# Kernel optimization log

Measured on AMD Instinct MI355X. Metric: run time of the kernel, lower is better.

Reference implementation:

```python
import jax, jax.numpy as jnp
import numpy as np

TAU = 2.0       # LIF membrane time constant (spikingjelly default)
ALPHA = 2.0     # ATan surrogate sharpness
EPS = 1e-5      # BN eps
NUM_HEADS = 12
PATCH = 2
LENTH = 256     # (H/PATCH)*(W/PATCH)

@jax.custom_vjp
def heaviside(x):
    return (x >= 0.0).astype(x.dtype)

def _hv_fwd(x):
    return heaviside(x), x

def _hv_bwd(x, g):
    sg = ALPHA / 2.0 / (1.0 + (jnp.pi / 2.0 * ALPHA * x) ** 2)  # ATan surrogate
    return (g * sg,)

heaviside.defvjp(_hv_fwd, _hv_bwd)

def lif(x):
    # multi-step LIF over leading time axis, hard reset, v_th = 1.0
    def step(v, xt):
        v = v + (xt - v) / TAU
        s = heaviside(v - 1.0)
        return v * (1.0 - s), s
    _, s = jax.lax.scan(step, jnp.zeros_like(x[0]), x)
    return s

def setup_inputs() -> dict:
    key = jax.random.key(0)
    ks = jax.random.split(key, 9)
    T, B, C, H, W = 4, 4, 384, 32, 32
    x = jax.random.normal(ks[0], (T, B, C, H, W), dtype=jnp.float32)
    Wconv = jax.random.normal(ks[1], (2 * C, C, PATCH, PATCH), dtype=jnp.float32) * (1.0 / np.sqrt(C * PATCH * PATCH))
    gamma1 = jax.random.uniform(ks[2], (2 * C,), dtype=jnp.float32, minval=0.5, maxval=1.5)
    beta1 = jax.random.normal(ks[3], (2 * C,), dtype=jnp.float32) * 0.1
    Wproj = jax.random.normal(ks[4], (C, C), dtype=jnp.float32) * (1.0 / np.sqrt(C))
    gamma2 = jax.random.uniform(ks[5], (C,), dtype=jnp.float32, minval=0.5, maxval=1.5)
    beta2 = jax.random.normal(ks[6], (C,), dtype=jnp.float32) * 0.1
    firing_rate_x = jax.random.uniform(ks[7], (1, 1, NUM_HEADS, 1, 1), dtype=jnp.float32, minval=0.05, maxval=0.5)
    firing_rate_attn = jax.random.uniform(ks[8], (1, 1, NUM_HEADS, 1, 1), dtype=jnp.float32, minval=0.05, maxval=0.5)
    return {"x": x, "Wconv": Wconv, "gamma1": gamma1, "beta1": beta1, "Wproj": Wproj,
            "gamma2": gamma2, "beta2": beta2, "firing_rate_x": firing_rate_x,
            "firing_rate_attn": firing_rate_attn}

def reference(x, Wconv, gamma1, beta1, Wproj, gamma2, beta2, firing_rate_x, firing_rate_attn):
    T, B, C, H, W = x.shape
    d = C // NUM_HEADS
    xs = lif(x)                                          # spikes [T,B,C,H,W]
    # patch conv dim -> 2*dim, stride = kernel = PATCH (eval BN: running mean 0, var 1)
    y = jax.lax.conv_general_dilated(xs.reshape(T * B, C, H, W), Wconv,
                                     (PATCH, PATCH), 'VALID',
                                     dimension_numbers=('NCHW', 'OIHW', 'NCHW'))
    bn1 = gamma1 / jnp.sqrt(1.0 + EPS)
    y = y * bn1[None, :, None, None] + beta1[None, :, None, None]
    Np = (H // PATCH) * (W // PATCH)                     # == LENTH
    y = y.reshape(T, B, NUM_HEADS, 2 * d, Np)
    y1, y2 = y[:, :, :, :d, :], y[:, :, :, d:, :]
    xr = xs.reshape(T, B, NUM_HEADS, d, H * W)
    scale1 = 1.0 / jnp.sqrt(firing_rate_x * d)
    attn = jnp.einsum('tbhdn,tbhdm->tbhnm', y1, xr) * scale1   # [T,B,h,Np,HW]
    attn = lif(attn)
    scale2 = 1.0 / jnp.sqrt(firing_rate_attn * LENTH)
    out = jnp.einsum('tbhdn,tbhnm->tbhdm', y2, attn) * scale2  # [T,B,h,d,HW]
    out = out.reshape(T, B, C, H, W)
    out = lif(out)
    out = jnp.einsum('oc,tbchw->tbohw', Wproj, out)            # 1x1 conv proj
    bn2 = gamma2 / jnp.sqrt(1.0 + EPS)
    out = out * bn2[None, None, :, None, None] + beta2[None, None, :, None, None]
    return out + x
```

## Files before the change

kernel.cpp:

```cpp
#include <hip/hip_runtime.h>
#include <hip/hip_bf16.h>
#include <math.h>


typedef __attribute__((ext_vector_type(8))) short short8;
typedef __attribute__((ext_vector_type(4))) float f32x4;

#define T_ 4
#define B_ 4
#define C_ 384
#define HW 1024
#define NH_ 12
#define Np_ 256
#define EPS_ 1e-5f
#define LDK 56

static __device__ __forceinline__ unsigned short f2bf(float f) {
    __hip_bfloat16 h = __float2bfloat16(f);
    return *reinterpret_cast<unsigned short*>(&h);
}
static __device__ __forceinline__ float bf2f(unsigned short u) {
    __hip_bfloat16 h = *reinterpret_cast<__hip_bfloat16*>(&u);
    return __bfloat162float(h);
}
static __device__ __forceinline__ void split3(float w, unsigned short& u0,
                                              unsigned short& u1, unsigned short& u2) {
    u0 = f2bf(w);  float f0 = bf2f(u0);
    float r1 = w - f0;
    u1 = f2bf(r1); float f1 = bf2f(u1);
    u2 = f2bf(r1 - f1);
}

__global__ __launch_bounds__(256) void k_wsplit(const float* __restrict__ Wc,
                                                const float* __restrict__ Wp,
                                                unsigned short* __restrict__ Wc3,
                                                unsigned short* __restrict__ Wp3) {
    const int NC = 768 * 1536;
    const int NP = 384 * 384;
    int i = blockIdx.x * 256 + threadIdx.x;
    float w; unsigned short* dst; int idx, plane;
    if (i < NC) { w = Wc[i]; dst = Wc3; idx = i; plane = NC; }
    else {
        int j = i - NC;
        if (j >= NP) return;
        w = Wp[j]; dst = Wp3; idx = j; plane = NP;
    }
    unsigned short u0, u1, u2;
    split3(w, u0, u1, u2);
    dst[idx] = u0; dst[plane + idx] = u1; dst[2 * plane + idx] = u2;
}

__global__ __launch_bounds__(256) void k_lif_im2col(const float* __restrict__ x,
                                                    unsigned short* __restrict__ Bc,
                                                    unsigned short* __restrict__ xsb) {
    int gt = blockIdx.x * 256 + threadIdx.x;
    int pw = gt & 15, ph = (gt >> 4) & 15;
    int v = gt >> 8;
    int c = v % 384, b = v / 384;
    float v00 = 0.f, v01 = 0.f, v10 = 0.f, v11 = 0.f;
    const size_t xrow = ((size_t)b * C_ + c) * HW + (size_t)(2 * ph) * 32 + 2 * pw;
#pragma unroll
    for (int t = 0; t < T_; ++t) {
        const float* px = x + (size_t)t * (B_ * C_ * HW) + xrow;
        float2 r0 = *(const float2*)px;
        float2 r1 = *(const float2*)(px + 32);
        v00 += (r0.x - v00) * 0.5f;
        v01 += (r0.y - v01) * 0.5f;
        v10 += (r1.x - v10) * 0.5f;
        v11 += (r1.y - v11) * 0.5f;
        ushort4 s;
        s.x = (v00 >= 1.f) ? 0x3F80 : 0; if (v00 >= 1.f) v00 = 0.f;
        s.y = (v01 >= 1.f) ? 0x3F80 : 0; if (v01 >= 1.f) v01 = 0.f;
        s.z = (v10 >= 1.f) ? 0x3F80 : 0; if (v10 >= 1.f) v10 = 0.f;
        s.w = (v11 >= 1.f) ? 0x3F80 : 0; if (v11 >= 1.f) v11 = 0.f;
        int tb = t * B_ + b;
        int n = tb * 256 + ph * 16 + pw;
        *(ushort4*)(Bc + (size_t)n * 1536 + 4 * c) = s;
        size_t xo = ((size_t)tb * C_ + c) * HW + (size_t)(2 * ph) * 32 + 2 * pw;
        ushort2 w0 = {s.x, s.y}, w1 = {s.z, s.w};
        *(ushort2*)(xsb + xo) = w0;
        *(ushort2*)(xsb + xo + 32) = w1;
    }
}

#define GL16(GP, LP) __builtin_amdgcn_global_load_lds(                        \
    (const __attribute__((address_space(1))) void*)(GP),                      \
    (__attribute__((address_space(3))) void*)(LP), 16, 0, 0)

static __device__ __forceinline__ void stage_conv(const unsigned short* __restrict__ Wc3,
                                                  const unsigned short* __restrict__ Bc,
                                                  short* smb, int mb, int nb, int k0,
                                                  int wid, int rloc, int cswz) {
    if (wid == 0) {
#pragma unroll
        for (int s = 0; s < 3; ++s)
#pragma unroll
            for (int u = 0; u < 2; ++u)
                GL16(Wc3 + ((size_t)(s * 768 + mb * 32 + u * 16 + rloc)) * 1536 + k0 + cswz * 8,
                     smb + s * 1024 + u * 512);
        GL16(Bc + ((size_t)(nb * 128 + rloc)) * 1536 + k0 + cswz * 8, smb + 3072);
    } else {
#pragma unroll
        for (int v = 1; v < 8; ++v)
            GL16(Bc + ((size_t)(nb * 128 + v * 16 + rloc)) * 1536 + k0 + cswz * 8,
                 smb + 3072 + v * 512);
    }
}

__global__ __launch_bounds__(128) void k_mconv(const unsigned short* __restrict__ Bc,
                                               const unsigned short* __restrict__ Wc3,
                                               const float* __restrict__ g1,
                                               const float* __restrict__ b1,
                                               const float* __restrict__ frx,
                                               const float* __restrict__ fra,
                                               unsigned short* __restrict__ y1s,
                                               unsigned short* __restrict__ y2s) {
    __shared__ short sm[2][7168];
    const int nb = blockIdx.x, mb = blockIdx.y;
    const int tid = threadIdx.x;
    const int lane = tid & 63, wid = tid >> 6;
    const int quad = lane >> 4, lr = lane & 15;
    const int rloc = lane >> 2;
    const int cswz = (lane & 3) ^ ((lane >> 3) & 3);
    const int slot = quad ^ ((lr >> 1) & 3);
    const int wn = wid;

    f32x4 acc[2][4];
#pragma unroll
    for (int im = 0; im < 2; ++im)
#pragma unroll
        for (int in = 0; in < 4; ++in)
            acc[im][in] = (f32x4){0.f, 0.f, 0.f, 0.f};

    stage_conv(Wc3, Bc, sm[0], mb, nb, 0, wid, rloc, cswz);

#pragma unroll 2
    for (int kt = 0; kt < 48; ++kt) {
        const int b = kt & 1;
        if (kt < 47) {
            stage_conv(Wc3, Bc, sm[b ^ 1], mb, nb, (kt + 1) * 32, wid, rloc, cswz);
            asm volatile("s_waitcnt vmcnt(7)" ::: "memory");
        } else {
            asm volatile("s_waitcnt vmcnt(0)" ::: "memory");
        }
        __builtin_amdgcn_s_barrier();
        __builtin_amdgcn_sched_barrier(0);

        const short* smb = sm[b];
        short8 af[3][2], bf[4];
#pragma unroll
        for (int s = 0; s < 3; ++s)
#pragma unroll
            for (int im = 0; im < 2; ++im)
                af[s][im] = *(const short8*)&smb[s * 1024 + (im * 16 + lr) * 32 + slot * 8];
#pragma unroll
        for (int in = 0; in < 4; ++in)
            bf[in] = *(const short8*)&smb[3072 + (wn * 64 + in * 16 + lr) * 32 + slot * 8];
        asm volatile("s_waitcnt lgkmcnt(0)" ::: "memory");
        __builtin_amdgcn_sched_barrier(0);
        __builtin_amdgcn_s_barrier();
        __builtin_amdgcn_sched_barrier(0);

#pragma unroll
        for (int s = 0; s < 3; ++s)
#pragma unroll
            for (int im = 0; im < 2; ++im)
#pragma unroll
                for (int in = 0; in < 4; ++in)
                    acc[im][in] = __builtin_amdgcn_mfma_f32_16x16x32_bf16(af[s][im], bf[in], acc[im][in], 0, 0, 0);
    }

    const float rs = 1.0f / sqrtf(1.0f + EPS_);
    const int h = mb >> 1, half = mb & 1;
    const float scl = (half == 0) ? (1.0f / sqrtf(frx[h] * 32.0f))
                                  : (1.0f / sqrtf(fra[h] * 256.0f));
    unsigned short* dst = (half == 0) ? y1s : y2s;
#pragma unroll
    for (int im = 0; im < 2; ++im) {
#pragma unroll
        for (int in = 0; in < 4; ++in) {
            int n_g = nb * 128 + wn * 64 + in * 16 + lr;
            int tb = n_g >> 8, pn = n_g & 255;
            size_t base = (size_t)(tb * NH_ + h) * 3 * 8192;
            ushort4 o0, o1, o2;
#pragma unroll
            for (int r = 0; r < 4; ++r) {
                int oc = mb * 32 + im * 16 + quad * 4 + r;
                float val = (acc[im][in][r] * (g1[oc] * rs) + b1[oc]) * scl;
                unsigned short u0, u1, u2;
                split3(val, u0, u1, u2);
                ((unsigned short*)&o0)[r] = u0;
                ((unsigned short*)&o1)[r] = u1;
                ((unsigned short*)&o2)[r] = u2;
            }
            int dd = im * 16 + quad * 4;
            if (half == 0) {
                *(ushort4*)&dst[base + 0 * 8192 + (size_t)pn * 32 + dd] = o0;
                *(ushort4*)&dst[base + 1 * 8192 + (size_t)pn * 32 + dd] = o1;
                *(ushort4*)&dst[base + 2 * 8192 + (size_t)pn * 32 + dd] = o2;
            } else {
#pragma unroll
                for (int r = 0; r < 4; ++r) {
                    dst[base + 0 * 8192 + (size_t)(dd + r) * 256 + pn] = ((unsigned short*)&o0)[r];
                    dst[base + 1 * 8192 + (size_t)(dd + r) * 256 + pn] = ((unsigned short*)&o1)[r];
                    dst[base + 2 * 8192 + (size_t)(dd + r) * 256 + pn] = ((unsigned short*)&o2)[r];
                }
            }
        }
    }
}

__global__ __launch_bounds__(256, 2) void k_attn_qk(const unsigned short* __restrict__ xsb,
                                                    const unsigned short* __restrict__ y1s,
                                                    unsigned short* __restrict__ abq) {
    __shared__ unsigned short xb[4][64][40];
    const int h = blockIdx.y, b = blockIdx.z;
    const int tid = threadIdx.x;
    const int lane = tid & 63, wq = tid >> 6;
    const int quad = lane >> 4, lr = lane & 15;
    const int m0 = blockIdx.x * 64;

#pragma unroll
    for (int i = 0; i < 8; ++i) {
        int e = tid + i * 256;
        int j4 = e & 15, d = (e >> 4) & 31, t = e >> 9;
        ushort4 v = *(const ushort4*)(xsb + ((size_t)((t * B_ + b) * C_) + h * 32 + d) * HW + m0 + j4 * 4);
        xb[t][j4 * 4 + 0][d] = v.x;
        xb[t][j4 * 4 + 1][d] = v.y;
        xb[t][j4 * 4 + 2][d] = v.z;
        xb[t][j4 * 4 + 3][d] = v.w;
    }
    __syncthreads();

    float vat[4][4][4];
#pragma unroll
    for (int mi = 0; mi < 4; ++mi)
#pragma unroll
        for (int itl = 0; itl < 4; ++itl)
#pragma unroll
            for (int r = 0; r < 4; ++r) vat[mi][itl][r] = 0.f;

#pragma unroll
    for (int t = 0; t < T_; ++t) {
        const int tb = t * B_ + b;
        const size_t slab = (size_t)(tb * NH_ + h) * 3 * 8192;

        short8 af[3][4];
        const unsigned short* y1p = y1s + slab + (size_t)(wq * 64 + lr) * 32 + quad * 8;
#pragma unroll
        for (int s = 0; s < 3; ++s)
#pragma unroll
            for (int itl = 0; itl < 4; ++itl)
                af[s][itl] = *(const short8*)(y1p + s * 8192 + itl * 512);

#pragma unroll
        for (int mi = 0; mi < 4; ++mi) {
            short8 bx = *(const short8*)&xb[t][mi * 16 + lr][quad * 8];
            f32x4 acc[4];
#pragma unroll
            for (int itl = 0; itl < 4; ++itl) acc[itl] = (f32x4){0.f, 0.f, 0.f, 0.f};
#pragma unroll
            for (int s = 0; s < 3; ++s)
#pragma unroll
                for (int itl = 0; itl < 4; ++itl)
                    acc[itl] = __builtin_amdgcn_mfma_f32_16x16x32_bf16(af[s][itl], bx, acc[itl], 0, 0, 0);

            unsigned int q = 0;
#pragma unroll
            for (int itl = 0; itl < 4; ++itl)
#pragma unroll
                for (int r = 0; r < 4; ++r) {
                    float v = vat[mi][itl][r];
                    v += (acc[itl][r] - v) * 0.5f;
                    bool s = (v >= 1.0f);
                    vat[mi][itl][r] = s ? 0.f : v;
                    q |= (s ? 1u : 0u) << (itl * 4 + r);
                }
            int m = m0 + mi * 16 + lr;
            abq[(((size_t)(tb * NH_ + h) * 1024 + m) * 4 + quad) * 4 + wq] = (unsigned short)q;
        }
    }
}

__global__ __launch_bounds__(128) void k_attn_pv(const unsigned long long* __restrict__ abits,
                                                 const unsigned short* __restrict__ y2s,
                                                 unsigned short* __restrict__ obt) {
    const int h = blockIdx.y, b = blockIdx.z;
    const int tid = threadIdx.x;
    const int lane = tid & 63;
    const int quad = lane >> 4, lr = lane & 15;
    const int dt = tid >> 6;
    const int mbase = blockIdx.x * 64;
    const int obase = (quad & 2) << 1;

    float vo[4][4];
#pragma unroll
    for (int mi = 0; mi < 4; ++mi)
#pragma unroll
        for (int r = 0; r < 4; ++r) vo[mi][r] = 0.f;

#pragma unroll
    for (int t = 0; t < T_; ++t) {
        const int tb = t * B_ + b;
        const size_t slab = (size_t)(tb * NH_ + h) * 3 * 8192;

        short8 ay[3][8];
        const unsigned short* y2p = y2s + slab + (size_t)(dt * 16 + lr) * 256 + quad * 8;
#pragma unroll
        for (int s = 0; s < 3; ++s)
#pragma unroll
            for (int kt = 0; kt < 8; ++kt)
                ay[s][kt] = *(const short8*)(y2p + s * 8192 + kt * 32);

#pragma unroll
        for (int mi = 0; mi < 4; ++mi) {
            const int m = mbase + mi * 16 + lr;
            const unsigned long long* ap = abits + ((size_t)(tb * NH_ + h) * 1024 + m) * 4 + (quad & 1) * 2;
            unsigned long long Qa = ap[0];
            unsigned long long Qb = ap[1];

            short8 bs[8];
#pragma unroll
            for (int kt = 0; kt < 8; ++kt) {
                int o = kt * 8 + obase;
                unsigned int a4 = (unsigned int)(Qa >> o) & 15u;
                unsigned int b4 = (unsigned int)(Qb >> o) & 15u;
                union { short8 v; unsigned int w[4]; } u;
                u.w[0] = ((a4 & 1u) ? 0x3F80u : 0u) | ((a4 & 2u) ? 0x3F800000u : 0u);
                u.w[1] = ((a4 & 4u) ? 0x3F80u : 0u) | ((a4 & 8u) ? 0x3F800000u : 0u);
                u.w[2] = ((b4 & 1u) ? 0x3F80u : 0u) | ((b4 & 2u) ? 0x3F800000u : 0u);
                u.w[3] = ((b4 & 4u) ? 0x3F80u : 0u) | ((b4 & 8u) ? 0x3F800000u : 0u);
                bs[kt] = u.v;
            }

            f32x4 acc2 = (f32x4){0.f, 0.f, 0.f, 0.f};
#pragma unroll
            for (int s = 0; s < 3; ++s)
#pragma unroll
                for (int kt = 0; kt < 8; ++kt)
                    acc2 = __builtin_amdgcn_mfma_f32_16x16x32_bf16(ay[s][kt], bs[kt], acc2, 0, 0, 0);

            ushort4 ob;
#pragma unroll
            for (int r = 0; r < 4; ++r) {
                float v = vo[mi][r];
                v += (acc2[r] - v) * 0.5f;
                bool s = (v >= 1.0f);
                ((unsigned short*)&ob)[r] = s ? 0x3F80 : 0;
                vo[mi][r] = s ? 0.f : v;
            }
            *(ushort4*)(obt + ((size_t)tb * HW + m) * C_ + h * 32 + dt * 16 + quad * 4) = ob;
        }
    }
}

__global__ __launch_bounds__(256) void k_mproj(const unsigned short* __restrict__ obt,
                                               const unsigned short* __restrict__ Wp3,
                                               const float* __restrict__ g2,
                                               const float* __restrict__ b2,
                                               const float* __restrict__ x,
                                               float* __restrict__ out) {
    __shared__ short As[3][64][LDK];
    __shared__ short Bs[128][LDK];
    const int nb = blockIdx.x, mb = blockIdx.y;
    const int tid = threadIdx.x;
    const int lane = tid & 63, wave = tid >> 6;
    const int wm = wave >> 1, wn = wave & 1;
    const int quad = lane >> 4, lr = lane & 15;
    const int arow = tid >> 2, akoff = (tid & 3) * 8;
    f32x4 acc[2][4];
#pragma unroll
    for (int im = 0; im < 2; ++im)
#pragma unroll
        for (int in = 0; in < 4; ++in)
            acc[im][in] = (f32x4){0.f, 0.f, 0.f, 0.f};

    for (int k0 = 0; k0 < 384; k0 += 32) {
#pragma unroll
        for (int s = 0; s < 3; ++s) {
            short8 a = *(const short8*)(Wp3 + ((size_t)(s * 384 + mb * 64 + arow)) * 384 + k0 + akoff);
            *(short8*)&As[s][arow][akoff] = a;
        }
#pragma unroll
        for (int i = 0; i < 2; ++i) {
            int f = i * 256 + tid;
            int row = f >> 2, koff = (f & 3) * 8;
            short8 bv = *(const short8*)(obt + ((size_t)(nb * 128 + row)) * 384 + k0 + koff);
            *(short8*)&Bs[row][koff] = bv;
        }
        __syncthreads();
        short8 bf[4], af[3][2];
#pragma unroll
        for (int in = 0; in < 4; ++in)
            bf[in] = *(const short8*)&Bs[wn * 64 + in * 16 + lr][quad * 8];
#pragma unroll
        for (int s = 0; s < 3; ++s)
#pragma unroll
            for (int im = 0; im < 2; ++im)
                af[s][im] = *(const short8*)&As[s][wm * 32 + im * 16 + lr][quad * 8];
#pragma unroll
        for (int s = 0; s < 3; ++s)
#pragma unroll
            for (int im = 0; im < 2; ++im)
#pragma unroll
                for (int in = 0; in < 4; ++in)
                    acc[im][in] = __builtin_amdgcn_mfma_f32_16x16x32_bf16(af[s][im], bf[in], acc[im][in], 0, 0, 0);
        __syncthreads();
    }
    const float rs = 1.0f / sqrtf(1.0f + EPS_);
#pragma unroll
    for (int im = 0; im < 2; ++im) {
#pragma unroll
        for (int in = 0; in < 4; ++in) {
            int n_g = nb * 128 + wn * 64 + in * 16 + lr;
            int tb = n_g >> 10, hw = n_g & 1023;
#pragma unroll
            for (int r = 0; r < 4; ++r) {
                int o = mb * 64 + wm * 32 + im * 16 + quad * 4 + r;
                size_t idx = ((size_t)tb * C_ + o) * HW + hw;
                out[idx] = acc[im][in][r] * (g2[o] * rs) + b2[o] + x[idx];
            }
        }
    }
}

extern "C" void kernel_launch(void* const* d_in, const int* in_sizes, int n_in,
                              void* d_out, int out_size, void* d_ws, size_t ws_size,
                              hipStream_t stream) {
    const float* x      = (const float*)d_in[0];
    const float* Wconv  = (const float*)d_in[1];
    const float* gamma1 = (const float*)d_in[2];
    const float* beta1  = (const float*)d_in[3];
    const float* Wproj  = (const float*)d_in[4];
    const float* gamma2 = (const float*)d_in[5];
    const float* beta2  = (const float*)d_in[6];
    const float* frx    = (const float*)d_in[7];
    const float* fra    = (const float*)d_in[8];
    float* out = (float*)d_out;

    unsigned short* ws16 = (unsigned short*)d_ws;
    unsigned short* Bc  = ws16;
    unsigned short* obt = ws16;
    unsigned short* Wc3 = ws16 + 6291456;
    unsigned short* Wp3 = ws16 + 9830400;
    unsigned short* xsb = ws16 + 10272768;
    unsigned short* y1s = ws16 + 16564224;
    unsigned short* y2s = ws16 + 21282816;
    unsigned long long* abits = (unsigned long long*)(ws16 + 26001408);

    k_wsplit<<<5184, 256, 0, stream>>>(Wconv, Wproj, Wc3, Wp3);
    k_lif_im2col<<<1536, 256, 0, stream>>>(x, Bc, xsb);
    k_mconv<<<dim3(32, 24), 128, 0, stream>>>(Bc, Wc3, gamma1, beta1, frx, fra, y1s, y2s);
    k_attn_qk<<<dim3(16, 12, 4), 256, 0, stream>>>(xsb, y1s, (unsigned short*)abits);
    k_attn_pv<<<dim3(16, 12, 4), 128, 0, stream>>>(abits, y2s, obt);
    k_mproj<<<dim3(128, 6), 256, 0, stream>>>(obt, Wp3, gamma2, beta2, x, out);
}
```

Measured before the change: 237.3 us.

## Double-buffer projection GEMM with direct global-to-LDS loads and swizzle QK tile

After: 242.5 us. 2.2% more time.

```diff
diff --git a/kernel.cpp b/kernel.cpp
--- a/kernel.cpp
+++ b/kernel.cpp
@@ -13,7 +13,6 @@
 #define NH_ 12
 #define Np_ 256
 #define EPS_ 1e-5f
-#define LDK 56
 
 static __device__ __forceinline__ unsigned short f2bf(float f) {
     __hip_bfloat16 h = __float2bfloat16(f);
@@ -225,10 +224,12 @@
         int e = tid + i * 256;
         int j4 = e & 15, d = (e >> 4) & 31, t = e >> 9;
         ushort4 v = *(const ushort4*)(xsb + ((size_t)((t * B_ + b) * C_) + h * 32 + d) * HW + m0 + j4 * 4);
-        xb[t][j4 * 4 + 0][d] = v.x;
-        xb[t][j4 * 4 + 1][d] = v.y;
-        xb[t][j4 * 4 + 2][d] = v.z;
-        xb[t][j4 * 4 + 3][d] = v.w;
+        int key = (j4 ^ (j4 >> 2)) & 3;
+        int cc = ((((d >> 3) ^ key) << 3) | (d & 7));
+        xb[t][j4 * 4 + 0][cc] = v.x;
+        xb[t][j4 * 4 + 1][cc] = v.y;
+        xb[t][j4 * 4 + 2][cc] = v.z;
+        xb[t][j4 * 4 + 3][cc] = v.w;
     }
     __syncthreads();
 
@@ -255,7 +256,8 @@
 
 #pragma unroll
         for (int mi = 0; mi < 4; ++mi) {
-            short8 bx = *(const short8*)&xb[t][mi * 16 + lr][quad * 8];
+            int keyr = ((lr >> 2) ^ mi) & 3;
+            short8 bx = *(const short8*)&xb[t][mi * 16 + lr][(quad ^ keyr) * 8];
             f32x4 acc[4];
 #pragma unroll
             for (int itl = 0; itl < 4; ++itl) acc[itl] = (f32x4){0.f, 0.f, 0.f, 0.f};
@@ -354,20 +356,41 @@
     }
 }
 
+static __device__ __forceinline__ void stage_proj(const unsigned short* __restrict__ Wp3,
+                                                  const unsigned short* __restrict__ obt,
+                                                  short* smb, int mb, int nb, int k0,
+                                                  int wid, int rloc, int cswz) {
+    if (wid < 3) {
+#pragma unroll
+        for (int u = 0; u < 4; ++u)
+            GL16(Wp3 + ((size_t)(wid * 384 + mb * 64 + u * 16 + rloc)) * 384 + k0 + cswz * 8,
+                 smb + wid * 2048 + u * 512);
+        GL16(obt + ((size_t)(nb * 128 + wid * 16 + rloc)) * 384 + k0 + cswz * 8,
+             smb + 6144 + wid * 512);
+    } else {
+#pragma unroll
+        for (int v = 3; v < 8; ++v)
+            GL16(obt + ((size_t)(nb * 128 + v * 16 + rloc)) * 384 + k0 + cswz * 8,
+                 smb + 6144 + v * 512);
+    }
+}
+
 __global__ __launch_bounds__(256) void k_mproj(const unsigned short* __restrict__ obt,
                                                const unsigned short* __restrict__ Wp3,
                                                const float* __restrict__ g2,
                                                const float* __restrict__ b2,
                                                const float* __restrict__ x,
                                                float* __restrict__ out) {
-    __shared__ short As[3][64][LDK];
-    __shared__ short Bs[128][LDK];
+    __shared__ short sm[2][10240];
     const int nb = blockIdx.x, mb = blockIdx.y;
     const int tid = threadIdx.x;
     const int lane = tid & 63, wave = tid >> 6;
     const int wm = wave >> 1, wn = wave & 1;
     const int quad = lane >> 4, lr = lane & 15;
-    const int arow = tid >> 2, akoff = (tid & 3) * 8;
+    const int rloc = lane >> 2;
+    const int cswz = (lane & 3) ^ ((lane >> 3) & 3);
+    const int slot = quad ^ ((lr >> 1) & 3);
+
     f32x4 acc[2][4];
 #pragma unroll
     for (int im = 0; im < 2; ++im)
@@ -375,29 +398,34 @@
         for (int in = 0; in < 4; ++in)
             acc[im][in] = (f32x4){0.f, 0.f, 0.f, 0.f};
 
-    for (int k0 = 0; k0 < 384; k0 += 32) {
-#pragma unroll
-        for (int s = 0; s < 3; ++s) {
-            short8 a = *(const short8*)(Wp3 + ((size_t)(s * 384 + mb * 64 + arow)) * 384 + k0 + akoff);
-            *(short8*)&As[s][arow][akoff] = a;
-        }
-#pragma unroll
-        for (int i = 0; i < 2; ++i) {
-            int f = i * 256 + tid;
-            int row = f >> 2, koff = (f & 3) * 8;
-            short8 bv = *(const short8*)(obt + ((size_t)(nb * 128 + row)) * 384 + k0 + koff);
-            *(short8*)&Bs[row][koff] = bv;
-        }
-        __syncthreads();
-        short8 bf[4], af[3][2];
+    stage_proj(Wp3, obt, sm[0], mb, nb, 0, wave, rloc, cswz);
+
+    for (int kt = 0; kt < 12; ++kt) {
+        const int b = kt & 1;
+        if (kt < 11) {
+            stage_proj(Wp3, obt, sm[b ^ 1], mb, nb, (kt + 1) * 32, wave, rloc, cswz);
+            asm volatile("s_waitcnt vmcnt(5)" ::: "memory");
+        } else {
+            asm volatile("s_waitcnt vmcnt(0)" ::: "memory");
+        }
+        __builtin_amdgcn_s_barrier();
+        __builtin_amdgcn_sched_barrier(0);
+
+        const short* smb = sm[b];
+        short8 af[3][2], bf[4];
+#pragma unroll
+        for (int s = 0; s < 3; ++s)
+#pragma unroll
+            for (int im = 0; im < 2; ++im)
+                af[s][im] = *(const short8*)&smb[s * 2048 + (wm * 32 + im * 16 + lr) * 32 + slot * 8];
 #pragma unroll
         for (int in = 0; in < 4; ++in)
-            bf[in] = *(const short8*)&Bs[wn * 64 + in * 16 + lr][quad * 8];
-#pragma unroll
-        for (int s = 0; s < 3; ++s)
-#pragma unroll
-            for (int im = 0; im < 2; ++im)
-                af[s][im] = *(const short8*)&As[s][wm * 32 + im * 16 + lr][quad * 8];
+            bf[in] = *(const short8*)&smb[6144 + (wn * 64 + in * 16 + lr) * 32 + slot * 8];
+        asm volatile("s_waitcnt lgkmcnt(0)" ::: "memory");
+        __builtin_amdgcn_sched_barrier(0);
+        __builtin_amdgcn_s_barrier();
+        __builtin_amdgcn_sched_barrier(0);
+
 #pragma unroll
         for (int s = 0; s < 3; ++s)
 #pragma unroll
@@ -405,8 +433,8 @@
 #pragma unroll
                 for (int in = 0; in < 4; ++in)
                     acc[im][in] = __builtin_amdgcn_mfma_f32_16x16x32_bf16(af[s][im], bf[in], acc[im][in], 0, 0, 0);
-        __syncthreads();
-    }
+    }
+
     const float rs = 1.0f / sqrtf(1.0f + EPS_);
 #pragma unroll
     for (int im = 0; im < 2; ++im) {
```
